# Optimization experiments

Hardware: AMD Instinct MI355X
Metric: run time of the kernel (lower is better)

Reference implementation:

```python
import jax, jax.numpy as jnp
import numpy as np

N = 50000
IN_CH = 64
HID_CH = 32
NEG_SLOPE = 0.2  # PyG GATConv default for attention LeakyReLU


def _glorot(key, shape):
    fan = shape[0] + shape[-1] if len(shape) > 1 else shape[0]
    s = jnp.sqrt(6.0 / fan)
    return jax.random.uniform(key, shape, jnp.float32, -s, s)


def setup_inputs() -> dict:
    key = jax.random.key(0)
    ks = jax.random.split(key, 20)
    x = jax.random.normal(ks[0], (N, IN_CH), jnp.float32)
    edge_index = jax.random.randint(ks[1], (2, 800000), 0, N, jnp.int64)
    dims = [(IN_CH, IN_CH), (IN_CH, HID_CH), (HID_CH, IN_CH), (IN_CH, IN_CH)]
    inp = {"x": x, "edge_index": edge_index}
    for i, (di, do) in enumerate(dims, 1):
        inp[f"w{i}"] = _glorot(ks[4 * i - 2], (di, do))
        inp[f"as{i}"] = _glorot(ks[4 * i - 1], (do,))
        inp[f"ad{i}"] = _glorot(ks[4 * i], (do,))
        inp[f"b{i}"] = jnp.zeros((do,), jnp.float32)
    return inp


def _gat_layer(x, src, dst, W, a_src, a_dst, b):
    # x: [N, di] -> h: [N, do]
    h = x @ W
    # per-edge attention logits (source + destination contributions)
    e = jax.nn.leaky_relu(h[src] @ a_src + h[dst] @ a_dst, NEG_SLOPE)  # [E]
    # numerically stable segment softmax over incoming edges per dst node
    m = jax.ops.segment_max(e, dst, num_segments=N)
    ex = jnp.exp(e - m[dst])
    denom = jax.ops.segment_sum(ex, dst, num_segments=N)
    alpha = ex / (denom[dst] + 1e-16)  # [E]
    out = jax.ops.segment_sum(alpha[:, None] * h[src], dst, num_segments=N)
    return out + b


def reference(x, edge_index, w1, as1, ad1, b1, w2, as2, ad2, b2,
              w3, as3, ad3, b3, w4, as4, ad4, b4):
    # PyG GATConv adds self-loops by default
    ar = jnp.arange(N, dtype=edge_index.dtype)
    src = jnp.concatenate([edge_index[0], ar])
    dst = jnp.concatenate([edge_index[1], ar])

    h1 = jax.nn.relu(_gat_layer(x, src, dst, w1, as1, ad1, b1))
    h = _gat_layer(h1, src, dst, w2, as2, ad2, b2)
    h3 = jax.nn.relu(h)
    h4 = jax.nn.relu(_gat_layer(h3, src, dst, w3, as3, ad3, b3))
    out = _gat_layer(h4, src, dst, w4, as4, ad4, b4)
    return (out, h)
```

## Files before the change

kernel.cpp:

```cpp
#include <hip/hip_runtime.h>
#include <hip/hip_fp16.h>
#include <math.h>

#define N_NODES 50000
#define N_EDGES 800000
#define E_TOT   850000
#define NEG_SLOPE 0.2f
#define NB_SCAN 49

typedef unsigned short u16;

__global__ void csr_init(int* deg) {
    int i = blockIdx.x * blockDim.x + threadIdx.x;
    if (i < N_NODES) deg[i] = 0;
}

__global__ void csr_degree(const int* __restrict__ dst, int* __restrict__ deg,
                           u16* __restrict__ rank) {
    int e = blockIdx.x * blockDim.x + threadIdx.x;
    if (e >= E_TOT) return;
    int d = (e < N_EDGES) ? dst[e] : (e - N_EDGES);
    rank[e] = (u16)atomicAdd(&deg[d], 1);
}

__global__ void scan_p1(const int* __restrict__ deg, int* __restrict__ bsum) {
    __shared__ int red[1024];
    int i = blockIdx.x * 1024 + threadIdx.x;
    red[threadIdx.x] = (i < N_NODES) ? deg[i] : 0;
    __syncthreads();
    for (int off = 512; off >= 1; off >>= 1) {
        if (threadIdx.x < off) red[threadIdx.x] += red[threadIdx.x + off];
        __syncthreads();
    }
    if (threadIdx.x == 0) bsum[blockIdx.x] = red[0];
}

__global__ void scan_p3(const int* __restrict__ deg, const int* __restrict__ bsum,
                        int* __restrict__ offs) {
    __shared__ int s[1024];
    __shared__ int bofs;
    int i = blockIdx.x * 1024 + threadIdx.x;
    int v = (i < N_NODES) ? deg[i] : 0;
    s[threadIdx.x] = v;
    if (threadIdx.x < 64) {
        int d = (threadIdx.x < NB_SCAN) ? bsum[threadIdx.x] : 0;
        int p = d;
        for (int off = 1; off < 64; off <<= 1) {
            int u = __shfl_up(p, off, 64);
            if ((int)threadIdx.x >= off) p += u;
        }
        if ((int)threadIdx.x == (int)blockIdx.x) bofs = p - d;
        if (blockIdx.x == NB_SCAN - 1 && threadIdx.x == NB_SCAN - 1)
            offs[N_NODES] = p;
    }
    __syncthreads();
    for (int off = 1; off < 1024; off <<= 1) {
        int u = (threadIdx.x >= off) ? s[threadIdx.x - off] : 0;
        __syncthreads();
        s[threadIdx.x] += u;
        __syncthreads();
    }
    if (i < N_NODES) offs[i] = bofs + s[threadIdx.x] - v;
}

__global__ void csr_fill(const int* __restrict__ src, const int* __restrict__ dst,
                         const u16* __restrict__ rank, const int* __restrict__ offs,
                         u16* __restrict__ csr_src) {
    int e = blockIdx.x * blockDim.x + threadIdx.x;
    if (e >= E_TOT) return;
    int s, d;
    if (e < N_EDGES) { s = src[e]; d = dst[e]; } else { s = e - N_EDGES; d = s; }
    csr_src[offs[d] + rank[e]] = (u16)s;
}

template<int DI, int DO>
__global__ void gemm_proj(const float* __restrict__ X, const float* __restrict__ W,
                          const float* __restrict__ a_src, const float* __restrict__ a_dst,
                          __half* __restrict__ Hh, float* __restrict__ ssrc,
                          float* __restrict__ sdst) {
    const int TPN = DO / 4;
    const int NPB = 256 / TPN;
    __shared__ float sW[DI * DO];
    __shared__ float sX[NPB][DI + 1];
    const int tid = threadIdx.x;
    for (int i = tid; i < DI * DO / 4; i += 256)
        ((float4*)sW)[i] = ((const float4*)W)[i];
    const int base = blockIdx.x * NPB;
    for (int i = tid; i < NPB * DI; i += 256) {
        int r = i / DI, col = i % DI;
        int node = base + r;
        sX[r][col] = (node < N_NODES) ? X[(long)node * DI + col] : 0.0f;
    }
    __syncthreads();
    const int cq = tid % TPN;
    const int g  = tid / TPN;
    const int node = base + g;
    if (node >= N_NODES) return;
    float ax = 0.0f, ay = 0.0f, az = 0.0f, aw = 0.0f;
    const float4* sW4 = (const float4*)sW;
#pragma unroll
    for (int k = 0; k < DI; k++) {
        float xv = sX[g][k];
        float4 w4 = sW4[k * TPN + cq];
        ax = fmaf(xv, w4.x, ax); ay = fmaf(xv, w4.y, ay);
        az = fmaf(xv, w4.z, az); aw = fmaf(xv, w4.w, aw);
    }
    union { uint2 u; __half2 h2[2]; } pk;
    pk.h2[0] = __float22half2_rn(make_float2(ax, ay));
    pk.h2[1] = __float22half2_rn(make_float2(az, aw));
    ((uint2*)(Hh + (long)node * DO))[cq] = pk.u;

    float4 as4 = ((const float4*)a_src)[cq];
    float4 ad4 = ((const float4*)a_dst)[cq];
    float ps = ax * as4.x + ay * as4.y + az * as4.z + aw * as4.w;
    float pd = ax * ad4.x + ay * ad4.y + az * ad4.z + aw * ad4.w;
#pragma unroll
    for (int m = TPN / 2; m >= 1; m >>= 1) {
        ps += __shfl_xor(ps, m, TPN);
        pd += __shfl_xor(pd, m, TPN);
    }
    if (cq == 0) { ssrc[node] = ps; sdst[node] = pd; }
}

template<int DIN, int DOUT>
__global__ void gather_gemm(const __half* __restrict__ Hh_in,
                            const float* __restrict__ ssrc_in,
                            const float* __restrict__ sdst_in,
                            const int* __restrict__ offs,
                            const u16* __restrict__ csr_src,
                            const float* __restrict__ bias_in,
                            int relu_o, float* __restrict__ extra_out,
                            const float* __restrict__ W2,
                            const float* __restrict__ a_src2,
                            const float* __restrict__ a_dst2,
                            __half* __restrict__ Hh_out,
                            float* __restrict__ ssrc2, float* __restrict__ sdst2) {
    const int G = DIN / 4;
    const int NPB = 256 / G;
    constexpr int LDSW = (DOUT > 0) ? DIN * DOUT : 1;
    __shared__ float sW[LDSW];
    if constexpr (DOUT > 0) {
        for (int i = threadIdx.x; i < DIN * DOUT / 4; i += 256)
            ((float4*)sW)[i] = ((const float4*)W2)[i];
        __syncthreads();
    }
    const int t = threadIdx.x;
    const int node = blockIdx.x * NPB + t / G;
    const int r = t % G;
    const bool valid = (node < N_NODES);
    const int beg = valid ? offs[node] : 0;
    const int end = valid ? offs[node + 1] : 0;
    const int deg = end - beg;
    const float sdv = valid ? sdst_in[node] : 0.0f;
    const uint2* H2 = (const uint2*)Hh_in;

    int   s0 = 0, s1 = 0;
    float ex0 = 0.0f, ex1 = 0.0f;
    if (r < deg)     s0 = csr_src[beg + r];
    if (G + r < deg) s1 = csr_src[beg + G + r];
    if (r < deg) {
        float v = ssrc_in[s0] + sdv;
        v = (v > 0.0f) ? v : NEG_SLOPE * v;
        ex0 = __expf(v);
    }
    if (G + r < deg) {
        float v = ssrc_in[s1] + sdv;
        v = (v > 0.0f) ? v : NEG_SLOPE * v;
        ex1 = __expf(v);
    }
    float den = ex0 + ex1;
    float4 acc = make_float4(0.0f, 0.0f, 0.0f, 0.0f);

#pragma unroll
    for (int j = 0; j < G; j++) {
        int   sa = __shfl(s0, j, G);
        float ea = __shfl(ex0, j, G);
        union { uint2 u; __half2 h2[2]; } ua;
        ua.u = H2[(long)sa * G + r];
        float2 a0 = __half22float2(ua.h2[0]), a1 = __half22float2(ua.h2[1]);
        acc.x = fmaf(ea, a0.x, acc.x); acc.y = fmaf(ea, a0.y, acc.y);
        acc.z = fmaf(ea, a1.x, acc.z); acc.w = fmaf(ea, a1.y, acc.w);
    }
    if (deg > G) {
#pragma unroll
        for (int j = 0; j < G; j++) {
            int   sa = __shfl(s1, j, G);
            float ea = __shfl(ex1, j, G);
            union { uint2 u; __half2 h2[2]; } ua;
            ua.u = H2[(long)sa * G + r];
            float2 a0 = __half22float2(ua.h2[0]), a1 = __half22float2(ua.h2[1]);
            acc.x = fmaf(ea, a0.x, acc.x); acc.y = fmaf(ea, a0.y, acc.y);
            acc.z = fmaf(ea, a1.x, acc.z); acc.w = fmaf(ea, a1.y, acc.w);
        }
    }
    for (int cb = beg + 2 * G; cb < end; cb += G) {
        int cnt = min(G, end - cb);
        int s2 = 0; float ex2 = 0.0f;
        if (r < cnt) {
            s2 = csr_src[cb + r];
            float v = ssrc_in[s2] + sdv;
            v = (v > 0.0f) ? v : NEG_SLOPE * v;
            ex2 = __expf(v);
        }
        den += ex2;
#pragma unroll
        for (int j = 0; j < G; j++) {
            int   sa = __shfl(s2, j, G);
            float ea = __shfl(ex2, j, G);
            union { uint2 u; __half2 h2[2]; } ua;
            ua.u = H2[(long)sa * G + r];
            float2 a0 = __half22float2(ua.h2[0]), a1 = __half22float2(ua.h2[1]);
            acc.x = fmaf(ea, a0.x, acc.x); acc.y = fmaf(ea, a0.y, acc.y);
            acc.z = fmaf(ea, a1.x, acc.z); acc.w = fmaf(ea, a1.y, acc.w);
        }
    }
#pragma unroll
    for (int m = G / 2; m >= 1; m >>= 1) den += __shfl_xor(den, m, G);

    float inv = 1.0f / (den + 1e-16f);
    float4 b4 = ((const float4*)bias_in)[r];
    float4 o;
    o.x = acc.x * inv + b4.x; o.y = acc.y * inv + b4.y;
    o.z = acc.z * inv + b4.z; o.w = acc.w * inv + b4.w;
    if (valid && extra_out) ((float4*)extra_out)[(long)node * G + r] = o;
    if (relu_o) {
        o.x = fmaxf(o.x, 0.0f); o.y = fmaxf(o.y, 0.0f);
        o.z = fmaxf(o.z, 0.0f); o.w = fmaxf(o.w, 0.0f);
    }

    if constexpr (DOUT > 0) {
        constexpr int C = DOUT / (DIN / 4);
        float acc2[C];
#pragma unroll
        for (int c = 0; c < C; c++) acc2[c] = 0.0f;
        const int cbase = r * C;
#pragma unroll
        for (int kb = 0; kb < G; kb++) {
            float4 o4;
            o4.x = __shfl(o.x, kb, G);
            o4.y = __shfl(o.y, kb, G);
            o4.z = __shfl(o.z, kb, G);
            o4.w = __shfl(o.w, kb, G);
            const float* wr = &sW[(4 * kb) * DOUT + cbase];
#pragma unroll
            for (int c = 0; c < C; c++) acc2[c] = fmaf(o4.x, wr[c], acc2[c]);
            wr += DOUT;
#pragma unroll
            for (int c = 0; c < C; c++) acc2[c] = fmaf(o4.y, wr[c], acc2[c]);
            wr += DOUT;
#pragma unroll
            for (int c = 0; c < C; c++) acc2[c] = fmaf(o4.z, wr[c], acc2[c]);
            wr += DOUT;
#pragma unroll
            for (int c = 0; c < C; c++) acc2[c] = fmaf(o4.w, wr[c], acc2[c]);
        }
        float ps = 0.0f, pd = 0.0f;
#pragma unroll
        for (int c = 0; c < C; c++) {
            ps = fmaf(acc2[c], a_src2[cbase + c], ps);
            pd = fmaf(acc2[c], a_dst2[cbase + c], pd);
        }
#pragma unroll
        for (int m = G / 2; m >= 1; m >>= 1) {
            ps += __shfl_xor(ps, m, G);
            pd += __shfl_xor(pd, m, G);
        }
        if (valid) {
            union { unsigned int u1; uint2 u2; uint4 u4; __half2 h[C / 2]; } pk;
#pragma unroll
            for (int c = 0; c < C; c += 2)
                pk.h[c / 2] = __float22half2_rn(make_float2(acc2[c], acc2[c + 1]));
            char* dp = (char*)(Hh_out + (long)node * DOUT + cbase);
            if constexpr (C == 2) *(unsigned int*)dp = pk.u1;
            else if constexpr (C == 4) *(uint2*)dp = pk.u2;
            else                        *(uint4*)dp = pk.u4;
            if (r == 0) { ssrc2[node] = ps; sdst2[node] = pd; }
        }
    }
}

extern "C" void kernel_launch(void* const* d_in, const int* in_sizes, int n_in,
                              void* d_out, int out_size, void* d_ws, size_t ws_size,
                              hipStream_t stream) {
    const float* x  = (const float*)d_in[0];
    const int*   ei = (const int*)d_in[1];

    const float* w1  = (const float*)d_in[2];
    const float* as1 = (const float*)d_in[3];
    const float* ad1 = (const float*)d_in[4];
    const float* b1  = (const float*)d_in[5];
    const float* w2  = (const float*)d_in[6];
    const float* as2 = (const float*)d_in[7];
    const float* ad2 = (const float*)d_in[8];
    const float* b2  = (const float*)d_in[9];
    const float* w3  = (const float*)d_in[10];
    const float* as3 = (const float*)d_in[11];
    const float* ad3 = (const float*)d_in[12];
    const float* b3  = (const float*)d_in[13];
    const float* w4  = (const float*)d_in[14];
    const float* as4 = (const float*)d_in[15];
    const float* ad4 = (const float*)d_in[16];
    const float* b4  = (const float*)d_in[17];

    float* out_final = (float*)d_out;
    float* out_h     = (float*)d_out + N_NODES * 64;

    float* ws    = (float*)d_ws;
    __half* Hh_a = (__half*)ws;
    __half* Hh_b = (__half*)(ws + N_NODES * 32);
    float* SS_a  = ws + 2 * N_NODES * 32;
    float* SD_a  = SS_a + N_NODES;
    float* SS_b  = SD_a + N_NODES;
    float* SD_b  = SS_b + N_NODES;
    int* deg     = (int*)(SD_b + N_NODES);
    u16* rank    = (u16*)(deg + N_NODES);
    int* offs    = (int*)(rank + E_TOT);
    u16* csr_src = (u16*)(offs + N_NODES + 1);
    int* bsum    = (int*)(csr_src + E_TOT);

    const int* src = ei;
    const int* dst = ei + N_EDGES;

    csr_init<<<(N_NODES + 255) / 256, 256, 0, stream>>>(deg);
    csr_degree<<<(E_TOT + 255) / 256, 256, 0, stream>>>(dst, deg, rank);
    scan_p1<<<NB_SCAN, 1024, 0, stream>>>(deg, bsum);
    scan_p3<<<NB_SCAN, 1024, 0, stream>>>(deg, bsum, offs);
    csr_fill<<<(E_TOT + 255) / 256, 256, 0, stream>>>(src, dst, rank, offs, csr_src);

    gemm_proj<64, 64><<<(N_NODES + 15) / 16, 256, 0, stream>>>(
        x, w1, as1, ad1, Hh_a, SS_a, SD_a);

    gather_gemm<64, 32><<<(N_NODES * 16 + 255) / 256, 256, 0, stream>>>(
        Hh_a, SS_a, SD_a, offs, csr_src, b1, 1, nullptr,
        w2, as2, ad2, Hh_b, SS_b, SD_b);
    gather_gemm<32, 64><<<(N_NODES * 8 + 255) / 256, 256, 0, stream>>>(
        Hh_b, SS_b, SD_b, offs, csr_src, b2, 1, out_h,
        w3, as3, ad3, Hh_a, SS_a, SD_a);
    gather_gemm<64, 64><<<(N_NODES * 16 + 255) / 256, 256, 0, stream>>>(
        Hh_a, SS_a, SD_a, offs, csr_src, b3, 1, nullptr,
        w4, as4, ad4, Hh_b, SS_b, SD_b);
    gather_gemm<64, 0><<<(N_NODES * 16 + 255) / 256, 256, 0, stream>>>(
        Hh_b, SS_b, SD_b, offs, csr_src, b4, 0, out_final,
        nullptr, nullptr, nullptr, nullptr, nullptr, nullptr);
}
```

Baseline: 272.1 us.

## Split 64-wide half features into two 32-wide planes gathered in separate passes

Stores each 64-channel fp16 feature matrix as two separate 32-channel planes and runs the gather for each plane in its own kernel pass. Each pass touches only a 3.2 MB working set, so the random neighbour gathers are more likely to stay in cache. The low-half result is staged in a float workspace (OL) and read back by the high-half pass, which performs the fused next-layer GEMM. The cost is recomputing the softmax weights twice per 64-wide layer, more kernel launches, and an extra round trip through global memory for the staged half.

```diff
diff --git a/kernel.cpp b/kernel.cpp
--- a/kernel.cpp
+++ b/kernel.cpp
@@ -7,6 +7,7 @@
 #define E_TOT   850000
 #define NEG_SLOPE 0.2f
 #define NB_SCAN 49
+#define PLANE   (N_NODES * 32)
 
 typedef unsigned short u16;
 
@@ -73,86 +74,85 @@
     csr_src[offs[d] + rank[e]] = (u16)s;
 }
 
-template<int DI, int DO>
 __global__ void gemm_proj(const float* __restrict__ X, const float* __restrict__ W,
                           const float* __restrict__ a_src, const float* __restrict__ a_dst,
                           __half* __restrict__ Hh, float* __restrict__ ssrc,
                           float* __restrict__ sdst) {
-    const int TPN = DO / 4;
-    const int NPB = 256 / TPN;
-    __shared__ float sW[DI * DO];
-    __shared__ float sX[NPB][DI + 1];
+    __shared__ float sW[64 * 64];
+    __shared__ float sX[16][65];
     const int tid = threadIdx.x;
-    for (int i = tid; i < DI * DO / 4; i += 256)
+    for (int i = tid; i < 64 * 64 / 4; i += 256)
         ((float4*)sW)[i] = ((const float4*)W)[i];
-    const int base = blockIdx.x * NPB;
-    for (int i = tid; i < NPB * DI; i += 256) {
-        int r = i / DI, col = i % DI;
+    const int base = blockIdx.x * 16;
+    for (int i = tid; i < 16 * 64; i += 256) {
+        int r = i / 64, col = i % 64;
         int node = base + r;
-        sX[r][col] = (node < N_NODES) ? X[(long)node * DI + col] : 0.0f;
+        sX[r][col] = (node < N_NODES) ? X[(long)node * 64 + col] : 0.0f;
     }
     __syncthreads();
-    const int cq = tid % TPN;
-    const int g  = tid / TPN;
+    const int cq = tid % 16;
+    const int g  = tid / 16;
     const int node = base + g;
     if (node >= N_NODES) return;
     float ax = 0.0f, ay = 0.0f, az = 0.0f, aw = 0.0f;
     const float4* sW4 = (const float4*)sW;
 #pragma unroll
-    for (int k = 0; k < DI; k++) {
+    for (int k = 0; k < 64; k++) {
         float xv = sX[g][k];
-        float4 w4 = sW4[k * TPN + cq];
+        float4 w4 = sW4[k * 16 + cq];
         ax = fmaf(xv, w4.x, ax); ay = fmaf(xv, w4.y, ay);
         az = fmaf(xv, w4.z, az); aw = fmaf(xv, w4.w, aw);
     }
     union { uint2 u; __half2 h2[2]; } pk;
     pk.h2[0] = __float22half2_rn(make_float2(ax, ay));
     pk.h2[1] = __float22half2_rn(make_float2(az, aw));
-    ((uint2*)(Hh + (long)node * DO))[cq] = pk.u;
+    __half* dp = (cq < 8) ? Hh + (long)node * 32 + 4 * cq
+                          : Hh + PLANE + (long)node * 32 + 4 * cq - 32;
+    *(uint2*)dp = pk.u;
 
     float4 as4 = ((const float4*)a_src)[cq];
     float4 ad4 = ((const float4*)a_dst)[cq];
     float ps = ax * as4.x + ay * as4.y + az * as4.z + aw * as4.w;
     float pd = ax * ad4.x + ay * ad4.y + az * ad4.z + aw * ad4.w;
 #pragma unroll
-    for (int m = TPN / 2; m >= 1; m >>= 1) {
-        ps += __shfl_xor(ps, m, TPN);
-        pd += __shfl_xor(pd, m, TPN);
+    for (int m = 8; m >= 1; m >>= 1) {
+        ps += __shfl_xor(ps, m, 16);
+        pd += __shfl_xor(pd, m, 16);
     }
     if (cq == 0) { ssrc[node] = ps; sdst[node] = pd; }
 }
 
-template<int DIN, int DOUT>
-__global__ void gather_gemm(const __half* __restrict__ Hh_in,
-                            const float* __restrict__ ssrc_in,
-                            const float* __restrict__ sdst_in,
-                            const int* __restrict__ offs,
-                            const u16* __restrict__ csr_src,
-                            const float* __restrict__ bias_in,
-                            int relu_o, float* __restrict__ extra_out,
-                            const float* __restrict__ W2,
-                            const float* __restrict__ a_src2,
-                            const float* __restrict__ a_dst2,
-                            __half* __restrict__ Hh_out,
-                            float* __restrict__ ssrc2, float* __restrict__ sdst2) {
-    const int G = DIN / 4;
-    const int NPB = 256 / G;
-    constexpr int LDSW = (DOUT > 0) ? DIN * DOUT : 1;
+template<int DOUT, int HI>
+__global__ void gather64(const __half* __restrict__ Hplane,
+                         const float* __restrict__ ssrc_in,
+                         const float* __restrict__ sdst_in,
+                         const int* __restrict__ offs,
+                         const u16* __restrict__ csr_src,
+                         const float* __restrict__ bias_in,
+                         int relu_o,
+                         float* __restrict__ extra_out,
+                         float* __restrict__ OL,
+                         const float* __restrict__ W2,
+                         const float* __restrict__ a_src2,
+                         const float* __restrict__ a_dst2,
+                         __half* __restrict__ Hh_out,
+                         float* __restrict__ ssrc2, float* __restrict__ sdst2) {
+    constexpr int G = 16;
+    constexpr bool DOGEMM = (DOUT > 0) && (HI == 1);
+    constexpr int LDSW = DOGEMM ? 64 * DOUT : 1;
     __shared__ float sW[LDSW];
-    if constexpr (DOUT > 0) {
-        for (int i = threadIdx.x; i < DIN * DOUT / 4; i += 256)
+    if constexpr (DOGEMM) {
+        for (int i = threadIdx.x; i < 64 * DOUT / 4; i += 256)
             ((float4*)sW)[i] = ((const float4*)W2)[i];
         __syncthreads();
     }
     const int t = threadIdx.x;
-    const int node = blockIdx.x * NPB + t / G;
+    const int node = blockIdx.x * 16 + t / G;
     const int r = t % G;
-    const bool valid = (node < N_NODES);
-    const int beg = valid ? offs[node] : 0;
-    const int end = valid ? offs[node + 1] : 0;
+    const int beg = offs[node], end = offs[node + 1];
     const int deg = end - beg;
-    const float sdv = valid ? sdst_in[node] : 0.0f;
-    const uint2* H2 = (const uint2*)Hh_in;
+    const float sdv = sdst_in[node];
+    const unsigned int* Hd = (const unsigned int*)Hplane;
 
     int   s0 = 0, s1 = 0;
     float ex0 = 0.0f, ex1 = 0.0f;
@@ -169,6 +169,152 @@
         ex1 = __expf(v);
     }
     float den = ex0 + ex1;
+    float2 acc = make_float2(0.0f, 0.0f);
+
+#pragma unroll
+    for (int j = 0; j < G; j++) {
+        int   sa = __shfl(s0, j, G);
+        float ea = __shfl(ex0, j, G);
+        unsigned int u = Hd[(long)sa * 16 + r];
+        float2 h = __half22float2(*(__half2*)&u);
+        acc.x = fmaf(ea, h.x, acc.x); acc.y = fmaf(ea, h.y, acc.y);
+    }
+    if (deg > G) {
+#pragma unroll
+        for (int j = 0; j < G; j++) {
+            int   sa = __shfl(s1, j, G);
+            float ea = __shfl(ex1, j, G);
+            unsigned int u = Hd[(long)sa * 16 + r];
+            float2 h = __half22float2(*(__half2*)&u);
+            acc.x = fmaf(ea, h.x, acc.x); acc.y = fmaf(ea, h.y, acc.y);
+        }
+    }
+    for (int cb = beg + 2 * G; cb < end; cb += G) {
+        int cnt = min(G, end - cb);
+        int s2 = 0; float ex2 = 0.0f;
+        if (r < cnt) {
+            s2 = csr_src[cb + r];
+            float v = ssrc_in[s2] + sdv;
+            v = (v > 0.0f) ? v : NEG_SLOPE * v;
+            ex2 = __expf(v);
+        }
+        den += ex2;
+#pragma unroll
+        for (int j = 0; j < G; j++) {
+            int   sa = __shfl(s2, j, G);
+            float ea = __shfl(ex2, j, G);
+            unsigned int u = Hd[(long)sa * 16 + r];
+            float2 h = __half22float2(*(__half2*)&u);
+            acc.x = fmaf(ea, h.x, acc.x); acc.y = fmaf(ea, h.y, acc.y);
+        }
+    }
+#pragma unroll
+    for (int m = G / 2; m >= 1; m >>= 1) den += __shfl_xor(den, m, G);
+
+    float inv = 1.0f / (den + 1e-16f);
+    float2 b2 = ((const float2*)bias_in)[HI * 16 + r];
+    float2 o;
+    o.x = acc.x * inv + b2.x; o.y = acc.y * inv + b2.y;
+    if (extra_out) ((float2*)(extra_out + (long)node * 64))[HI * 16 + r] = o;
+    if (relu_o) { o.x = fmaxf(o.x, 0.0f); o.y = fmaxf(o.y, 0.0f); }
+
+    if constexpr (DOUT > 0) {
+        if constexpr (HI == 0) {
+            ((float2*)OL)[(long)node * 16 + r] = o;
+        } else {
+            float2 olo = ((const float2*)OL)[(long)node * 16 + r];
+            constexpr int C = DOUT / 16;
+            float acc2[C];
+#pragma unroll
+            for (int c = 0; c < C; c++) acc2[c] = 0.0f;
+            const int cbase = r * C;
+#pragma unroll
+            for (int kb = 0; kb < 16; kb++) {
+                float lx = __shfl(olo.x, kb, G), ly = __shfl(olo.y, kb, G);
+                float hx = __shfl(o.x,  kb, G), hy = __shfl(o.y,  kb, G);
+                const float* w0 = &sW[(2 * kb) * DOUT + cbase];
+                const float* w1 = w0 + DOUT;
+                const float* w2 = &sW[(32 + 2 * kb) * DOUT + cbase];
+                const float* w3 = w2 + DOUT;
+#pragma unroll
+                for (int c = 0; c < C; c++) acc2[c] = fmaf(lx, w0[c], acc2[c]);
+#pragma unroll
+                for (int c = 0; c < C; c++) acc2[c] = fmaf(ly, w1[c], acc2[c]);
+#pragma unroll
+                for (int c = 0; c < C; c++) acc2[c] = fmaf(hx, w2[c], acc2[c]);
+#pragma unroll
+                for (int c = 0; c < C; c++) acc2[c] = fmaf(hy, w3[c], acc2[c]);
+            }
+            float ps = 0.0f, pd = 0.0f;
+#pragma unroll
+            for (int c = 0; c < C; c++) {
+                ps = fmaf(acc2[c], a_src2[cbase + c], ps);
+                pd = fmaf(acc2[c], a_dst2[cbase + c], pd);
+            }
+#pragma unroll
+            for (int m = G / 2; m >= 1; m >>= 1) {
+                ps += __shfl_xor(ps, m, G);
+                pd += __shfl_xor(pd, m, G);
+            }
+            union { unsigned int u1; uint2 u2; __half2 h[C / 2]; } pk;
+#pragma unroll
+            for (int c = 0; c < C; c += 2)
+                pk.h[c / 2] = __float22half2_rn(make_float2(acc2[c], acc2[c + 1]));
+            if constexpr (C == 4) {
+                __half* dp = (r < 8) ? Hh_out + (long)node * 32 + 4 * r
+                                     : Hh_out + PLANE + (long)node * 32 + 4 * r - 32;
+                *(uint2*)dp = pk.u2;
+            } else {
+                __half* dp = Hh_out + (long)node * 32 + 2 * r;
+                *(unsigned int*)dp = pk.u1;
+            }
+            if (r == 0) { ssrc2[node] = ps; sdst2[node] = pd; }
+        }
+    }
+}
+
+__global__ void gather32(const __half* __restrict__ Hh_in,
+                         const float* __restrict__ ssrc_in,
+                         const float* __restrict__ sdst_in,
+                         const int* __restrict__ offs,
+                         const u16* __restrict__ csr_src,
+                         const float* __restrict__ bias_in,
+                         float* __restrict__ extra_out,
+                         const float* __restrict__ W2,
+                         const float* __restrict__ a_src2,
+                         const float* __restrict__ a_dst2,
+                         __half* __restrict__ Hh_out,
+                         float* __restrict__ ssrc2, float* __restrict__ sdst2) {
+    const int G = 8;
+    __shared__ float sW[32 * 64];
+    for (int i = threadIdx.x; i < 32 * 64 / 4; i += 256)
+        ((float4*)sW)[i] = ((const float4*)W2)[i];
+    __syncthreads();
+    const int t = threadIdx.x;
+    const int node = blockIdx.x * 32 + t / G;
+    const int r = t % G;
+    const bool valid = (node < N_NODES);
+    const int beg = valid ? offs[node] : 0;
+    const int end = valid ? offs[node + 1] : 0;
+    const int deg = end - beg;
+    const float sdv = valid ? sdst_in[node] : 0.0f;
+    const uint2* H2 = (const uint2*)Hh_in;
+
+    int   s0 = 0, s1 = 0;
+    float ex0 = 0.0f, ex1 = 0.0f;
+    if (r < deg)     s0 = csr_src[beg + r];
+    if (G + r < deg) s1 = csr_src[beg + G + r];
+    if (r < deg) {
+        float v = ssrc_in[s0] + sdv;
+        v = (v > 0.0f) ? v : NEG_SLOPE * v;
+        ex0 = __expf(v);
+    }
+    if (G + r < deg) {
+        float v = ssrc_in[s1] + sdv;
+        v = (v > 0.0f) ? v : NEG_SLOPE * v;
+        ex1 = __expf(v);
+    }
+    float den = ex0 + ex1;
     float4 acc = make_float4(0.0f, 0.0f, 0.0f, 0.0f);
 
 #pragma unroll
@@ -223,59 +369,53 @@
     o.x = acc.x * inv + b4.x; o.y = acc.y * inv + b4.y;
     o.z = acc.z * inv + b4.z; o.w = acc.w * inv + b4.w;
     if (valid && extra_out) ((float4*)extra_out)[(long)node * G + r] = o;
-    if (relu_o) {
-        o.x = fmaxf(o.x, 0.0f); o.y = fmaxf(o.y, 0.0f);
-        o.z = fmaxf(o.z, 0.0f); o.w = fmaxf(o.w, 0.0f);
-    }
-
-    if constexpr (DOUT > 0) {
-        constexpr int C = DOUT / (DIN / 4);
-        float acc2[C];
-#pragma unroll
-        for (int c = 0; c < C; c++) acc2[c] = 0.0f;
-        const int cbase = r * C;
-#pragma unroll
-        for (int kb = 0; kb < G; kb++) {
-            float4 o4;
-            o4.x = __shfl(o.x, kb, G);
-            o4.y = __shfl(o.y, kb, G);
-            o4.z = __shfl(o.z, kb, G);
-            o4.w = __shfl(o.w, kb, G);
-            const float* wr = &sW[(4 * kb) * DOUT + cbase];
-#pragma unroll
-            for (int c = 0; c < C; c++) acc2[c] = fmaf(o4.x, wr[c], acc2[c]);
-            wr += DOUT;
-#pragma unroll
-            for (int c = 0; c < C; c++) acc2[c] = fmaf(o4.y, wr[c], acc2[c]);
-            wr += DOUT;
-#pragma unroll
-            for (int c = 0; c < C; c++) acc2[c] = fmaf(o4.z, wr[c], acc2[c]);
-            wr += DOUT;
-#pragma unroll
-            for (int c = 0; c < C; c++) acc2[c] = fmaf(o4.w, wr[c], acc2[c]);
-        }
-        float ps = 0.0f, pd = 0.0f;
-#pragma unroll
-        for (int c = 0; c < C; c++) {
-            ps = fmaf(acc2[c], a_src2[cbase + c], ps);
-            pd = fmaf(acc2[c], a_dst2[cbase + c], pd);
-        }
-#pragma unroll
-        for (int m = G / 2; m >= 1; m >>= 1) {
-            ps += __shfl_xor(ps, m, G);
-            pd += __shfl_xor(pd, m, G);
-        }
-        if (valid) {
-            union { unsigned int u1; uint2 u2; uint4 u4; __half2 h[C / 2]; } pk;
-#pragma unroll
-            for (int c = 0; c < C; c += 2)
-                pk.h[c / 2] = __float22half2_rn(make_float2(acc2[c], acc2[c + 1]));
-            char* dp = (char*)(Hh_out + (long)node * DOUT + cbase);
-            if constexpr (C == 2) *(unsigned int*)dp = pk.u1;
-            else if constexpr (C == 4) *(uint2*)dp = pk.u2;
-            else                        *(uint4*)dp = pk.u4;
-            if (r == 0) { ssrc2[node] = ps; sdst2[node] = pd; }
-        }
+    o.x = fmaxf(o.x, 0.0f); o.y = fmaxf(o.y, 0.0f);
+    o.z = fmaxf(o.z, 0.0f); o.w = fmaxf(o.w, 0.0f);
+
+    float acc2[8];
+#pragma unroll
+    for (int c = 0; c < 8; c++) acc2[c] = 0.0f;
+    const int cbase = r * 8;
+#pragma unroll
+    for (int kb = 0; kb < G; kb++) {
+        float4 o4;
+        o4.x = __shfl(o.x, kb, G);
+        o4.y = __shfl(o.y, kb, G);
+        o4.z = __shfl(o.z, kb, G);
+        o4.w = __shfl(o.w, kb, G);
+        const float* wr = &sW[(4 * kb) * 64 + cbase];
+#pragma unroll
+        for (int c = 0; c < 8; c++) acc2[c] = fmaf(o4.x, wr[c], acc2[c]);
+        wr += 64;
+#pragma unroll
+        for (int c = 0; c < 8; c++) acc2[c] = fmaf(o4.y, wr[c], acc2[c]);
+        wr += 64;
+#pragma unroll
+        for (int c = 0; c < 8; c++) acc2[c] = fmaf(o4.z, wr[c], acc2[c]);
+        wr += 64;
+#pragma unroll
+        for (int c = 0; c < 8; c++) acc2[c] = fmaf(o4.w, wr[c], acc2[c]);
+    }
+    float ps = 0.0f, pd = 0.0f;
+#pragma unroll
+    for (int c = 0; c < 8; c++) {
+        ps = fmaf(acc2[c], a_src2[cbase + c], ps);
+        pd = fmaf(acc2[c], a_dst2[cbase + c], pd);
+    }
+#pragma unroll
+    for (int m = G / 2; m >= 1; m >>= 1) {
+        ps += __shfl_xor(ps, m, G);
+        pd += __shfl_xor(pd, m, G);
+    }
+    if (valid) {
+        union { uint4 u4; __half2 h[4]; } pk;
+#pragma unroll
+        for (int c = 0; c < 8; c += 2)
+            pk.h[c / 2] = __float22half2_rn(make_float2(acc2[c], acc2[c + 1]));
+        __half* dp = (r < 4) ? Hh_out + (long)node * 32 + 8 * r
+                             : Hh_out + PLANE + (long)node * 32 + 8 * r - 32;
+        *(uint4*)dp = pk.u4;
+        if (r == 0) { ssrc2[node] = ps; sdst2[node] = pd; }
     }
 }
 
@@ -312,7 +452,8 @@
     float* SD_a  = SS_a + N_NODES;
     float* SS_b  = SD_a + N_NODES;
     float* SD_b  = SS_b + N_NODES;
-    int* deg     = (int*)(SD_b + N_NODES);
+    float* OL    = SD_b + N_NODES;
+    int* deg     = (int*)(OL + N_NODES * 32);
     u16* rank    = (u16*)(deg + N_NODES);
     int* offs    = (int*)(rank + E_TOT);
     u16* csr_src = (u16*)(offs + N_NODES + 1);
@@ -327,19 +468,31 @@
     scan_p3<<<NB_SCAN, 1024, 0, stream>>>(deg, bsum, offs);
     csr_fill<<<(E_TOT + 255) / 256, 256, 0, stream>>>(src, dst, rank, offs, csr_src);
 
-    gemm_proj<64, 64><<<(N_NODES + 15) / 16, 256, 0, stream>>>(
+    gemm_proj<<<(N_NODES + 15) / 16, 256, 0, stream>>>(
         x, w1, as1, ad1, Hh_a, SS_a, SD_a);
 
-    gather_gemm<64, 32><<<(N_NODES * 16 + 255) / 256, 256, 0, stream>>>(
-        Hh_a, SS_a, SD_a, offs, csr_src, b1, 1, nullptr,
+    const int GB64 = N_NODES / 16;
+    const int GB32 = (N_NODES + 31) / 32;
+
+    gather64<32, 0><<<GB64, 256, 0, stream>>>(
+        Hh_a, SS_a, SD_a, offs, csr_src, b1, 1, nullptr, OL,
         w2, as2, ad2, Hh_b, SS_b, SD_b);
-    gather_gemm<32, 64><<<(N_NODES * 8 + 255) / 256, 256, 0, stream>>>(
-        Hh_b, SS_b, SD_b, offs, csr_src, b2, 1, out_h,
+    gather64<32, 1><<<GB64, 256, 0, stream>>>(
+        Hh_a + PLANE, SS_a, SD_a, offs, csr_src, b1, 1, nullptr, OL,
+        w2, as2, ad2, Hh_b, SS_b, SD_b);
+    gather32<<<GB32, 256, 0, stream>>>(
+        Hh_b, SS_b, SD_b, offs, csr_src, b2, out_h,
         w3, as3, ad3, Hh_a, SS_a, SD_a);
-    gather_gemm<64, 64><<<(N_NODES * 16 + 255) / 256, 256, 0, stream>>>(
-        Hh_a, SS_a, SD_a, offs, csr_src, b3, 1, nullptr,
+    gather64<64, 0><<<GB64, 256, 0, stream>>>(
+        Hh_a, SS_a, SD_a, offs, csr_src, b3, 1, nullptr, OL,
         w4, as4, ad4, Hh_b, SS_b, SD_b);
-    gather_gemm<64, 0><<<(N_NODES * 16 + 255) / 256, 256, 0, stream>>>(
-        Hh_b, SS_b, SD_b, offs, csr_src, b4, 0, out_final,
+    gather64<64, 1><<<GB64, 256, 0, stream>>>(
+        Hh_a + PLANE, SS_a, SD_a, offs, csr_src, b3, 1, nullptr, OL,
+        w4, as4, ad4, Hh_b, SS_b, SD_b);
+    gather64<0, 0><<<GB64, 256, 0, stream>>>(
+        Hh_b, SS_b, SD_b, offs, csr_src, b4, 0, out_final, nullptr,
         nullptr, nullptr, nullptr, nullptr, nullptr, nullptr);
-}
+    gather64<0, 1><<<GB64, 256, 0, stream>>>(
+        Hh_b + PLANE, SS_b, SD_b, offs, csr_src, b4, 0, out_final, nullptr,
+        nullptr, nullptr, nullptr, nullptr, nullptr, nullptr);
+}
```

Result: slower. 303.8 us (+11.6%).

## Fuse CSR build into one persistent kernel with grid-wide barriers

Applied to the files above, without the earlier changes.

Replaces the five CSR construction kernels (init, degree, two-pass scan, fill) with one 512-block persistent kernel that separates the phases with atomic-counter grid barriers, plus a memset that zeroes the degrees and barrier counters. The aim is to cut several kernel launch gaps and tail effects on a small preprocessing stage. In exchange, correctness depends on all 512 blocks being co-resident, and spin-wait barriers add latency. The edge loops now use grid-stride iteration over fewer threads.

```diff
diff --git a/kernel.cpp b/kernel.cpp
--- a/kernel.cpp
+++ b/kernel.cpp
@@ -6,71 +6,100 @@
 #define N_EDGES 800000
 #define E_TOT   850000
 #define NEG_SLOPE 0.2f
-#define NB_SCAN 49
+#define PLANE   (N_NODES * 32)
+#define CB      512
+#define CHUNK   98
 
 typedef unsigned short u16;
 
-__global__ void csr_init(int* deg) {
-    int i = blockIdx.x * blockDim.x + threadIdx.x;
-    if (i < N_NODES) deg[i] = 0;
-}
-
-__global__ void csr_degree(const int* __restrict__ dst, int* __restrict__ deg,
-                           u16* __restrict__ rank) {
-    int e = blockIdx.x * blockDim.x + threadIdx.x;
-    if (e >= E_TOT) return;
-    int d = (e < N_EDGES) ? dst[e] : (e - N_EDGES);
-    rank[e] = (u16)atomicAdd(&deg[d], 1);
-}
-
-__global__ void scan_p1(const int* __restrict__ deg, int* __restrict__ bsum) {
-    __shared__ int red[1024];
-    int i = blockIdx.x * 1024 + threadIdx.x;
-    red[threadIdx.x] = (i < N_NODES) ? deg[i] : 0;
+__device__ __forceinline__ void gbar(int* bar, int target) {
     __syncthreads();
-    for (int off = 512; off >= 1; off >>= 1) {
-        if (threadIdx.x < off) red[threadIdx.x] += red[threadIdx.x + off];
+    if (threadIdx.x == 0) {
+        __threadfence();
+        atomicAdd(bar, 1);
+        while (__hip_atomic_load(bar, __ATOMIC_ACQUIRE, __HIP_MEMORY_SCOPE_AGENT)
+               < target) {
+            __builtin_amdgcn_s_sleep(8);
+        }
+    }
+    __syncthreads();
+}
+
+__global__ __launch_bounds__(256)
+void csr_build(const int* __restrict__ src, const int* __restrict__ dst,
+               int* __restrict__ deg, u16* __restrict__ rank,
+               int* __restrict__ offs, u16* __restrict__ csr_src,
+               int* __restrict__ bsum, int* __restrict__ bar) {
+    __shared__ int red[256];
+    const int tid = threadIdx.x;
+
+    for (int e = blockIdx.x * 256 + tid; e < E_TOT; e += CB * 256) {
+        int d;
+        if (e < N_EDGES) d = dst[e]; else d = e - N_EDGES;
+        rank[e] = (u16)atomicAdd(&deg[d], 1);
+    }
+    gbar(&bar[0], CB);
+
+    {
+        const int base = blockIdx.x * CHUNK;
+        int v = 0;
+        for (int i = tid; i < CHUNK; i += 256) {
+            int n = base + i;
+            if (n < N_NODES) v += deg[n];
+        }
+        red[tid] = v;
         __syncthreads();
-    }
-    if (threadIdx.x == 0) bsum[blockIdx.x] = red[0];
-}
-
-__global__ void scan_p3(const int* __restrict__ deg, const int* __restrict__ bsum,
-                        int* __restrict__ offs) {
-    __shared__ int s[1024];
-    __shared__ int bofs;
-    int i = blockIdx.x * 1024 + threadIdx.x;
-    int v = (i < N_NODES) ? deg[i] : 0;
-    s[threadIdx.x] = v;
-    if (threadIdx.x < 64) {
-        int d = (threadIdx.x < NB_SCAN) ? bsum[threadIdx.x] : 0;
-        int p = d;
-        for (int off = 1; off < 64; off <<= 1) {
-            int u = __shfl_up(p, off, 64);
-            if ((int)threadIdx.x >= off) p += u;
-        }
-        if ((int)threadIdx.x == (int)blockIdx.x) bofs = p - d;
-        if (blockIdx.x == NB_SCAN - 1 && threadIdx.x == NB_SCAN - 1)
-            offs[N_NODES] = p;
-    }
-    __syncthreads();
-    for (int off = 1; off < 1024; off <<= 1) {
-        int u = (threadIdx.x >= off) ? s[threadIdx.x - off] : 0;
+        for (int off = 128; off >= 1; off >>= 1) {
+            if (tid < off) red[tid] += red[tid + off];
+            __syncthreads();
+        }
+        if (tid == 0) bsum[blockIdx.x] = red[0];
+    }
+    gbar(&bar[1], CB);
+
+    if (blockIdx.x == 0) {
+        int b0 = bsum[2 * tid], b1 = bsum[2 * tid + 1];
+        int s = b0 + b1;
+        red[tid] = s;
         __syncthreads();
-        s[threadIdx.x] += u;
+        for (int off = 1; off < 256; off <<= 1) {
+            int u = (tid >= off) ? red[tid - off] : 0;
+            __syncthreads();
+            red[tid] += u;
+            __syncthreads();
+        }
+        int ex = red[tid] - s;
+        bsum[2 * tid] = ex;
+        bsum[2 * tid + 1] = ex + b0;
+        if (tid == 255) offs[N_NODES] = red[255];
+    }
+    gbar(&bar[2], CB);
+
+    {
+        __shared__ int sc[128];
+        const int base = blockIdx.x * CHUNK;
+        int v = 0;
+        if (tid < 128) {
+            v = (tid < CHUNK && base + tid < N_NODES) ? deg[base + tid] : 0;
+            sc[tid] = v;
+        }
         __syncthreads();
-    }
-    if (i < N_NODES) offs[i] = bofs + s[threadIdx.x] - v;
-}
-
-__global__ void csr_fill(const int* __restrict__ src, const int* __restrict__ dst,
-                         const u16* __restrict__ rank, const int* __restrict__ offs,
-                         u16* __restrict__ csr_src) {
-    int e = blockIdx.x * blockDim.x + threadIdx.x;
-    if (e >= E_TOT) return;
-    int s, d;
-    if (e < N_EDGES) { s = src[e]; d = dst[e]; } else { s = e - N_EDGES; d = s; }
-    csr_src[offs[d] + rank[e]] = (u16)s;
+        for (int off = 1; off < 128; off <<= 1) {
+            int u = (tid < 128 && tid >= off) ? sc[tid - off] : 0;
+            __syncthreads();
+            if (tid < 128) sc[tid] += u;
+            __syncthreads();
+        }
+        if (tid < CHUNK && base + tid < N_NODES)
+            offs[base + tid] = bsum[blockIdx.x] + sc[tid] - v;
+    }
+    gbar(&bar[3], CB);
+
+    for (int e = blockIdx.x * 256 + tid; e < E_TOT; e += CB * 256) {
+        int s, d;
+        if (e < N_EDGES) { s = src[e]; d = dst[e]; } else { s = e - N_EDGES; d = s; }
+        csr_src[offs[d] + rank[e]] = (u16)s;
+    }
 }
 
 template<int DI, int DO>
@@ -313,7 +342,8 @@
     float* SS_b  = SD_a + N_NODES;
     float* SD_b  = SS_b + N_NODES;
     int* deg     = (int*)(SD_b + N_NODES);
-    u16* rank    = (u16*)(deg + N_NODES);
+    int* bar     = deg + N_NODES;
+    u16* rank    = (u16*)(bar + 4);
     int* offs    = (int*)(rank + E_TOT);
     u16* csr_src = (u16*)(offs + N_NODES + 1);
     int* bsum    = (int*)(csr_src + E_TOT);
@@ -321,11 +351,8 @@
     const int* src = ei;
     const int* dst = ei + N_EDGES;
 
-    csr_init<<<(N_NODES + 255) / 256, 256, 0, stream>>>(deg);
-    csr_degree<<<(E_TOT + 255) / 256, 256, 0, stream>>>(dst, deg, rank);
-    scan_p1<<<NB_SCAN, 1024, 0, stream>>>(deg, bsum);
-    scan_p3<<<NB_SCAN, 1024, 0, stream>>>(deg, bsum, offs);
-    csr_fill<<<(E_TOT + 255) / 256, 256, 0, stream>>>(src, dst, rank, offs, csr_src);
+    hipMemsetAsync(deg, 0, (N_NODES + 4) * sizeof(int), stream);
+    csr_build<<<CB, 256, 0, stream>>>(src, dst, deg, rank, offs, csr_src, bsum, bar);
 
     gemm_proj<64, 64><<<(N_NODES + 15) / 16, 256, 0, stream>>>(
         x, w1, as1, ad1, Hh_a, SS_a, SD_a);
```

After: 437.4 us. 60.7% more time.
